# Optimization experiments

Hardware: AMD Instinct MI355X
Metric: run time of the kernel (lower is better)

Reference implementation:

```python
import jax, jax.numpy as jnp
import numpy as np

E, H, M, IN, T = 4, 64, 64, 32, 32      # e_size, hidden_state, message, in_size, target
HL = (128, 256, 128)                     # NNet hidden layers (priba's NNet default)
N_LAYERS = 3


def setup_inputs() -> dict:
    key = jax.random.key(0)
    ks = iter(jax.random.split(key, 64))
    B, N = 16, 128

    def w(shape, scale=0.1):
        return jax.random.normal(next(ks), shape, dtype=jnp.float32) * scale

    inp = {
        "h_in": jax.random.normal(next(ks), (B, N, IN), dtype=jnp.float32),
        "am": jax.random.normal(next(ks), (B, N, N, E), dtype=jnp.float32),
        "g_size": jax.random.randint(next(ks), (B,), 0, N),
    }
    # EdgeNetwork NNet: E -> 128 -> 256 -> 128 -> M*H
    dims_e = (E,) + HL + (M * H,)
    for i in range(4):
        inp[f"We{i}"] = w((dims_e[i], dims_e[i + 1]))
        inp[f"be{i}"] = w((dims_e[i + 1],))
    # GRU (torch nn.GRU, one layer, one step): input M, hidden H
    inp["Wih"] = w((3 * H, M)); inp["Whh"] = w((3 * H, H))
    inp["bih"] = w((3 * H,)); inp["bhh"] = w((3 * H,))
    # Readout NNets: i on [h_T, h_0] (H+IN -> T), j on h_T (H -> T)
    dims_i = (H + IN,) + HL + (T,)
    dims_j = (H,) + HL + (T,)
    for i in range(4):
        inp[f"Wi{i}"] = w((dims_i[i], dims_i[i + 1])); inp[f"bi{i}"] = w((dims_i[i + 1],))
        inp[f"Wj{i}"] = w((dims_j[i], dims_j[i + 1])); inp[f"bj{i}"] = w((dims_j[i + 1],))
    return inp


def _mlp(x, Ws, bs):
    for Wk, bk in zip(Ws[:-1], bs[:-1]):
        x = jax.nn.relu(x @ Wk + bk)
    return x @ Ws[-1] + bs[-1]


def reference(h_in, am, g_size,
              We0, be0, We1, be1, We2, be2, We3, be3,
              Wih, Whh, bih, bhh,
              Wi0, bi0, Wi1, bi1, Wi2, bi2, Wi3, bi3,
              Wj0, bj0, Wj1, bj1, Wj2, bj2, Wj3, bj3):
    B, N, _ = h_in.shape
    h = jnp.pad(h_in, ((0, 0), (0, 0), (0, H - IN)))            # pad to hidden size
    mask = (jnp.arange(N)[None, :] < g_size[:, None]).astype(h.dtype)[:, :, None]  # [B,N,1]

    # Edge-network hidden features; final linear layer is fused into the
    # message contraction to avoid materializing per-edge [M,H] matrices.
    f = am                                                       # [B,N,N,E]
    for Wk, bk in ((We0, be0), (We1, be1), (We2, be2)):
        f = jax.nn.relu(f @ Wk + bk)                             # [B,N,N,128]
    W3 = We3.reshape(HL[-1], M, H)                               # [128,M,H]
    b3 = be3.reshape(M, H)

    for _ in range(N_LAYERS):                                    # weight-tied GGNN steps
        # m[b,v,o] = sum_w (A(e_bvw) @ h_bw)[o], A = reshape(f @ We3 + be3)
        t = jnp.einsum('bvwk,bwi->bvki', f, h)                   # [B,N,128,H]
        msg = jnp.einsum('bvki,koi->bvo', t, W3)
        msg = msg + jnp.einsum('oi,bi->bo', b3, h.sum(1))[:, None, :]
        # single-step torch GRU update
        gi = msg @ Wih.T + bih
        gh = h @ Whh.T + bhh
        r = jax.nn.sigmoid(gi[..., :H] + gh[..., :H])
        z = jax.nn.sigmoid(gi[..., H:2 * H] + gh[..., H:2 * H])
        n = jnp.tanh(gi[..., 2 * H:] + r * gh[..., 2 * H:])
        h = (1.0 - z) * n + z * h
        h = h * mask

    # GGNN readout: sum_v mask * sigmoid(i([h_T, h_0])) * j(h_T), then log_softmax
    gate = jax.nn.sigmoid(_mlp(jnp.concatenate([h, h_in], -1),
                               (Wi0, Wi1, Wi2, Wi3), (bi0, bi1, bi2, bi3)))
    val = _mlp(h, (Wj0, Wj1, Wj2, Wj3), (bj0, bj1, bj2, bj3))
    res = (mask * gate * val).sum(1)                             # [B,T]
    return jax.nn.log_softmax(res, axis=1)
```

## Files before the change

### kernel.cpp

```cpp
#include <hip/hip_runtime.h>
#include <math.h>

#define B   16
#define N   128
#define E   4
#define H   64
#define M   64
#define IN_ 32
#define T   32
#define K1  128
#define K2  256
#define K3  128

typedef _Float16 f16;
typedef f16  f16x8 __attribute__((ext_vector_type(8)));
typedef f16  f16x4 __attribute__((ext_vector_type(4)));
typedef f16  f16x2 __attribute__((ext_vector_type(2)));
typedef float f32x4 __attribute__((ext_vector_type(4)));

#define MFMA16(a, b, c) __builtin_amdgcn_mfma_f32_16x16x32_f16(a, b, c, 0, 0, 0)

#define OFF_W1T   0
#define OFF_W2T   32768
#define OFF_WE3H  65536
#define OFF_RI0   589824
#define OFF_RI1   602112
#define OFF_RI2   634880
#define OFF_RI3   667648
#define OFF_RJ0   671744
#define OFF_RJ1   679936
#define OFF_RJ2   712704
#define OFF_RJ3   745472
#define WPACK_SZ  749568

union SmemU {
    struct { float xl[64][4]; f16 y1[64][136]; f16 y2[64][264]; } e;
    union {
        struct { f16 Al[128][72]; f16 Bl[128][72]; } in;
        f16 Ol[128][136];
    } pg;
    struct { float prt[4][64]; float hsum[64]; float bias[64]; } bi;
};

__global__ __launch_bounds__(256) void prep_kernel(
    const float* __restrict__ h_in,
    const float* __restrict__ We1, const float* __restrict__ We2,
    const float* __restrict__ We3,
    const float* __restrict__ Wi0, const float* __restrict__ Wi1,
    const float* __restrict__ Wi2, const float* __restrict__ Wi3,
    const float* __restrict__ Wj0, const float* __restrict__ Wj1,
    const float* __restrict__ Wj2, const float* __restrict__ Wj3,
    float* __restrict__ h, f16* __restrict__ h16, f16* __restrict__ hin16,
    f16* __restrict__ wp) {
    int idx = blockIdx.x * 256 + threadIdx.x;
    if (idx < B * N * H) {
        int i  = idx & (H - 1);
        int bn = idx >> 6;
        float v = (i < IN_) ? h_in[bn * IN_ + i] : 0.f;
        h[idx] = v;
        h16[idx] = (f16)v;
        if (i < IN_) hin16[bn * IN_ + i] = (f16)v;
    }
    if (idx >= WPACK_SZ) return;
    if (idx < OFF_W2T) {
        int j = idx >> 7, k = idx & 127;
        wp[idx] = (f16)We1[k * 256 + j];
    } else if (idx < OFF_WE3H) {
        int t = idx - OFF_W2T;
        int j = t >> 8, k = t & 255;
        wp[idx] = (f16)We2[k * 128 + j];
    } else if (idx < OFF_RI0) {
        wp[idx] = (f16)We3[idx - OFF_WE3H];
    } else if (idx < OFF_RI1) {
        int t = idx - OFF_RI0;
        int n = t / 96, c = t % 96;
        wp[idx] = (f16)Wi0[c * 128 + n];
    } else if (idx < OFF_RI2) {
        int t = idx - OFF_RI1;
        int n = t >> 7, k = t & 127;
        wp[idx] = (f16)Wi1[k * 256 + n];
    } else if (idx < OFF_RI3) {
        int t = idx - OFF_RI2;
        int n = t >> 8, k = t & 255;
        wp[idx] = (f16)Wi2[k * 128 + n];
    } else if (idx < OFF_RJ0) {
        int t = idx - OFF_RI3;
        int n = t >> 7, k = t & 127;
        wp[idx] = (f16)Wi3[k * 32 + n];
    } else if (idx < OFF_RJ1) {
        int t = idx - OFF_RJ0;
        int n = t >> 6, c = t & 63;
        wp[idx] = (f16)Wj0[c * 128 + n];
    } else if (idx < OFF_RJ2) {
        int t = idx - OFF_RJ1;
        int n = t >> 7, k = t & 127;
        wp[idx] = (f16)Wj1[k * 256 + n];
    } else if (idx < OFF_RJ3) {
        int t = idx - OFF_RJ2;
        int n = t >> 8, k = t & 255;
        wp[idx] = (f16)Wj2[k * 128 + n];
    } else {
        int t = idx - OFF_RJ3;
        int n = t >> 7, k = t & 127;
        wp[idx] = (f16)Wj3[k * 32 + n];
    }
}


__device__ void edge_body(SmemU& su, int tid, int tile,
                          const float* __restrict__ am,
                          const float* __restrict__ We0,
                          const float* __restrict__ be0,
                          const f16* __restrict__ W1t,
                          const float* __restrict__ be1,
                          const f16* __restrict__ W2t,
                          const float* __restrict__ be2,
                          f16* __restrict__ f) {
    int lane = tid & 63, wv = tid >> 6;
    long long g0 = (long long)tile * 64;

    ((float*)su.e.xl)[tid] = am[g0 * 4 + tid];
    __syncthreads();

    {
        int j0 = (tid & 63) * 2, e0 = (tid >> 6) * 16;
        float w00 = We0[j0],       w01 = We0[j0 + 1];
        float w10 = We0[128 + j0], w11 = We0[128 + j0 + 1];
        float w20 = We0[256 + j0], w21 = We0[256 + j0 + 1];
        float w30 = We0[384 + j0], w31 = We0[384 + j0 + 1];
        float b0 = be0[j0], b1 = be0[j0 + 1];
        #pragma unroll 4
        for (int e = e0; e < e0 + 16; ++e) {
            float x0 = su.e.xl[e][0], x1 = su.e.xl[e][1];
            float x2 = su.e.xl[e][2], x3 = su.e.xl[e][3];
            float v0 = b0 + x0 * w00 + x1 * w10 + x2 * w20 + x3 * w30;
            float v1 = b1 + x0 * w01 + x1 * w11 + x2 * w21 + x3 * w31;
            f16x2 p;
            p[0] = (f16)fmaxf(v0, 0.f);
            p[1] = (f16)fmaxf(v1, 0.f);
            *(f16x2*)&su.e.y1[e][j0] = p;
        }
    }
    __syncthreads();

    int m = lane & 15, q = lane >> 4;

    {
        f32x4 acc[4][4];
        #pragma unroll
        for (int ct = 0; ct < 4; ++ct)
            #pragma unroll
            for (int rt = 0; rt < 4; ++rt) acc[ct][rt] = (f32x4){0.f, 0.f, 0.f, 0.f};
        #pragma unroll
        for (int s = 0; s < 4; ++s) {
            int k0 = s * 32 + q * 8;
            f16x8 afr[4], bfr[4];
            #pragma unroll
            for (int rt = 0; rt < 4; ++rt)
                afr[rt] = *(const f16x8*)&su.e.y1[rt * 16 + m][k0];
            #pragma unroll
            for (int ct = 0; ct < 4; ++ct) {
                int n = (wv * 4 + ct) * 16 + m;
                bfr[ct] = *(const f16x8*)(W1t + n * 128 + k0);
            }
            #pragma unroll
            for (int ct = 0; ct < 4; ++ct)
                #pragma unroll
                for (int rt = 0; rt < 4; ++rt)
                    acc[ct][rt] = MFMA16(bfr[ct], afr[rt], acc[ct][rt]);
        }
        #pragma unroll
        for (int ct = 0; ct < 4; ++ct) {
            int n0 = (wv * 4 + ct) * 16 + q * 4;
            f32x4 bb = *(const f32x4*)&be1[n0];
            #pragma unroll
            for (int rt = 0; rt < 4; ++rt) {
                int e = rt * 16 + m;
                f16x4 pk;
                #pragma unroll
                for (int r = 0; r < 4; ++r)
                    pk[r] = (f16)fmaxf(acc[ct][rt][r] + bb[r], 0.f);
                *(f16x4*)&su.e.y2[e][n0] = pk;
            }
        }
    }
    __syncthreads();

    {
        f32x4 acc[2][4];
        #pragma unroll
        for (int ct = 0; ct < 2; ++ct)
            #pragma unroll
            for (int rt = 0; rt < 4; ++rt) acc[ct][rt] = (f32x4){0.f, 0.f, 0.f, 0.f};
        #pragma unroll
        for (int s = 0; s < 8; ++s) {
            int k0 = s * 32 + q * 8;
            f16x8 afr[4], bfr[2];
            #pragma unroll
            for (int rt = 0; rt < 4; ++rt)
                afr[rt] = *(const f16x8*)&su.e.y2[rt * 16 + m][k0];
            #pragma unroll
            for (int ct = 0; ct < 2; ++ct) {
                int n = (wv * 2 + ct) * 16 + m;
                bfr[ct] = *(const f16x8*)(W2t + n * 256 + k0);
            }
            #pragma unroll
            for (int ct = 0; ct < 2; ++ct)
                #pragma unroll
                for (int rt = 0; rt < 4; ++rt)
                    acc[ct][rt] = MFMA16(bfr[ct], afr[rt], acc[ct][rt]);
        }
        #pragma unroll
        for (int ct = 0; ct < 2; ++ct) {
            int n0 = (wv * 2 + ct) * 16 + q * 4;
            f32x4 bb = *(const f32x4*)&be2[n0];
            #pragma unroll
            for (int rt = 0; rt < 4; ++rt) {
                int e = rt * 16 + m;
                f16x4 pk;
                #pragma unroll
                for (int r = 0; r < 4; ++r)
                    pk[r] = (f16)fmaxf(acc[ct][rt][r] + bb[r], 0.f);
                *(f16x4*)&su.e.y1[e][n0] = pk;
            }
        }
    }
    __syncthreads();

    #pragma unroll
    for (int j = 0; j < 4; ++j) {
        int c = tid + j * 256;
        int e = c >> 4, pp = c & 15;
        *(uint4*)(f + (g0 + e) * 128 + pp * 8) = *(const uint4*)&su.e.y1[e][pp * 8];
    }
}

__device__ void pgemm_body(SmemU& su, int tid, int ob, int nt,
                           const f16* __restrict__ h16,
                           const f16* __restrict__ We3h,
                           f16* __restrict__ P2) {
    int lane = tid & 63, wv = tid >> 6;

    #pragma unroll
    for (int j = 0; j < 4; ++j) {
        int c = tid + j * 256;
        int row = c >> 3, pp = c & 7;
        *(uint4*)&su.pg.in.Al[row][pp * 8] =
            *(const uint4*)(h16 + (size_t)(nt * 128 + row) * 64 + pp * 8);
    }
    #pragma unroll
    for (int j = 0; j < 4; ++j) {
        int c = tid + j * 256;
        int k = c >> 3, pp = c & 7;
        *(uint4*)&su.pg.in.Bl[k][pp * 8] =
            *(const uint4*)(We3h + ((size_t)(k * 64 + ob)) * 64 + pp * 8);
    }
    __syncthreads();

    int m = lane & 15, q = lane >> 4;
    f32x4 acc[2][8];
    #pragma unroll
    for (int ct = 0; ct < 2; ++ct)
        #pragma unroll
        for (int rt = 0; rt < 8; ++rt) acc[ct][rt] = (f32x4){0.f, 0.f, 0.f, 0.f};
    #pragma unroll
    for (int s = 0; s < 2; ++s) {
        int k0 = s * 32 + q * 8;
        f16x8 afr[8], bfr[2];
        #pragma unroll
        for (int rt = 0; rt < 8; ++rt)
            afr[rt] = *(const f16x8*)&su.pg.in.Al[rt * 16 + m][k0];
        #pragma unroll
        for (int ct = 0; ct < 2; ++ct)
            bfr[ct] = *(const f16x8*)&su.pg.in.Bl[(wv * 2 + ct) * 16 + m][k0];
        #pragma unroll
        for (int ct = 0; ct < 2; ++ct)
            #pragma unroll
            for (int rt = 0; rt < 8; ++rt)
                acc[ct][rt] = MFMA16(bfr[ct], afr[rt], acc[ct][rt]);
    }
    __syncthreads();
    #pragma unroll
    for (int ct = 0; ct < 2; ++ct) {
        int c0 = (wv * 2 + ct) * 16 + q * 4;
        #pragma unroll
        for (int rt = 0; rt < 8; ++rt) {
            int v = rt * 16 + m;
            f16x4 pk;
            #pragma unroll
            for (int r = 0; r < 4; ++r) pk[r] = (f16)acc[ct][rt][r];
            *(f16x4*)&su.pg.Ol[v][c0] = pk;
        }
    }
    __syncthreads();
    #pragma unroll
    for (int j = 0; j < 8; ++j) {
        int c = tid + j * 256;
        int row = c >> 4, pp = c & 15;
        *(uint4*)(P2 + ((size_t)(nt * 128 + row) * 64 + ob) * 128 + pp * 8) =
            *(const uint4*)&su.pg.Ol[row][pp * 8];
    }
}

__device__ void bias_body(SmemU& su, int tid, int b,
                          const float* __restrict__ h,
                          const float* __restrict__ be3,
                          float* __restrict__ biasb) {
    int i = tid & 63, wq = tid >> 6;
    float s = 0.f;
    for (int w = wq; w < N; w += 4) s += h[((size_t)(b * N + w)) * H + i];
    su.bi.prt[wq][i] = s;
    __syncthreads();
    if (tid < 64)
        su.bi.hsum[tid] = su.bi.prt[0][tid] + su.bi.prt[1][tid]
                        + su.bi.prt[2][tid] + su.bi.prt[3][tid];
    __syncthreads();
    if (tid < 64) {
        float sb = 0.f;
        #pragma unroll 4
        for (int ii = 0; ii < H; ++ii) sb += be3[tid * H + ii] * su.bi.hsum[ii];
        biasb[b * 64 + tid] = sb;
    }
}

__global__ __launch_bounds__(256, 3) void mega0_kernel(
    const float* __restrict__ am,
    const float* __restrict__ We0, const float* __restrict__ be0,
    const float* __restrict__ be1, const float* __restrict__ be2,
    const float* __restrict__ be3,
    const f16* __restrict__ wp,
    const float* __restrict__ h, const f16* __restrict__ h16,
    f16* __restrict__ f, f16* __restrict__ P2, float* __restrict__ biasb) {
    __shared__ SmemU su;
    int tid = threadIdx.x;
    int bid = blockIdx.x;
    if (bid < 4096) {
        edge_body(su, tid, bid, am, We0, be0, wp + OFF_W1T, be1, wp + OFF_W2T,
                  be2, f);
    } else if (bid < 5120) {
        int t = bid - 4096;
        pgemm_body(su, tid, t & 63, t >> 6, h16, wp + OFF_WE3H, P2);
    } else {
        bias_body(su, tid, bid - 5120, h, be3, biasb);
    }
}

__global__ __launch_bounds__(256, 3) void pg_bias_kernel(
    const float* __restrict__ be3, const f16* __restrict__ wp,
    const float* __restrict__ h, const f16* __restrict__ h16,
    f16* __restrict__ P2, float* __restrict__ biasb) {
    __shared__ SmemU su;
    int tid = threadIdx.x;
    int bid = blockIdx.x;
    if (bid < 1024) {
        pgemm_body(su, tid, bid & 63, bid >> 6, h16, wp + OFF_WE3H, P2);
    } else {
        bias_body(su, tid, bid - 1024, h, be3, biasb);
    }
}

__global__ __launch_bounds__(256, 2) void msg_mfma(
    const f16* __restrict__ f, const f16* __restrict__ P2,
    float* __restrict__ part) {
    __shared__ f16 Al[128][136];
    __shared__ f16 Bl[64][136];
    int tid = threadIdx.x, lane = tid & 63, wv = tid >> 6;
    int ws = blockIdx.x;
    int b  = blockIdx.y;
    int m = lane & 15, q = lane >> 4;

    f32x4 acc[2][4];
    #pragma unroll
    for (int rt = 0; rt < 2; ++rt)
        #pragma unroll
        for (int ct = 0; ct < 4; ++ct) acc[rt][ct] = (f32x4){0.f, 0.f, 0.f, 0.f};

    for (int wi = 0; wi < 4; ++wi) {
        int w = ws * 4 + wi;
        #pragma unroll
        for (int j = 0; j < 8; ++j) {
            int c = tid + j * 256;
            int v = c >> 4, pp = c & 15;
            *(uint4*)&Al[v][pp * 8] =
                *(const uint4*)(f + (((size_t)(b * 128 + v) * 128 + w) * 128) + pp * 8);
        }
        #pragma unroll
        for (int j = 0; j < 4; ++j) {
            int c = tid + j * 256;
            int o = c >> 4, pp = c & 15;
            *(uint4*)&Bl[o][pp * 8] =
                *(const uint4*)(P2 + (((size_t)(b * 128 + w) * 64 + o) * 128) + pp * 8);
        }
        __syncthreads();
        #pragma unroll
        for (int s = 0; s < 4; ++s) {
            int k0 = s * 32 + q * 8;
            f16x8 afr[2], bfr[4];
            #pragma unroll
            for (int rt = 0; rt < 2; ++rt)
                afr[rt] = *(const f16x8*)&Al[(wv * 2 + rt) * 16 + m][k0];
            #pragma unroll
            for (int ct = 0; ct < 4; ++ct)
                bfr[ct] = *(const f16x8*)&Bl[ct * 16 + m][k0];
            #pragma unroll
            for (int rt = 0; rt < 2; ++rt)
                #pragma unroll
                for (int ct = 0; ct < 4; ++ct)
                    acc[rt][ct] = MFMA16(afr[rt], bfr[ct], acc[rt][ct]);
        }
        __syncthreads();
    }
    float* pp = part + (size_t)ws * (2048 * 64);
    #pragma unroll
    for (int rt = 0; rt < 2; ++rt)
        #pragma unroll
        for (int ct = 0; ct < 4; ++ct) {
            int o = ct * 16 + m;
            #pragma unroll
            for (int r = 0; r < 4; ++r) {
                int v = (wv * 2 + rt) * 16 + q * 4 + r;
                pp[(size_t)(b * 128 + v) * 64 + o] = acc[rt][ct][r];
            }
        }
}

__global__ __launch_bounds__(192) void gru_kernel(
    const float* __restrict__ biasb, const float* __restrict__ part,
    float* __restrict__ h, f16* __restrict__ h16,
    const float* __restrict__ Wih, const float* __restrict__ Whh,
    const float* __restrict__ bih, const float* __restrict__ bhh,
    const int* __restrict__ g_size) {
    __shared__ float m_lds[M];
    __shared__ float h_lds[H];
    __shared__ float gi[3 * H], gh[3 * H];
    int tid = threadIdx.x;
    int bv  = blockIdx.x;
    int b = bv >> 7, v = bv & 127;

    if (tid < M) {
        float s = biasb[b * 64 + tid];
        #pragma unroll 8
        for (int sp = 0; sp < 32; ++sp)
            s += part[(size_t)sp * (2048 * 64) + bv * 64 + tid];
        m_lds[tid] = s;
    } else if (tid < M + H) {
        h_lds[tid - M] = h[bv * H + (tid - M)];
    }
    __syncthreads();

    {
        float si = bih[tid], sh = bhh[tid];
        const float* wi = Wih + tid * M;
        const float* wh = Whh + tid * H;
        #pragma unroll 4
        for (int k = 0; k < M; ++k) si += wi[k] * m_lds[k];
        #pragma unroll 4
        for (int k = 0; k < H; ++k) sh += wh[k] * h_lds[k];
        gi[tid] = si;
        gh[tid] = sh;
    }
    __syncthreads();
    if (tid < H) {
        float r = 1.f / (1.f + expf(-(gi[tid] + gh[tid])));
        float z = 1.f / (1.f + expf(-(gi[H + tid] + gh[H + tid])));
        float n = tanhf(gi[2 * H + tid] + r * gh[2 * H + tid]);
        float hv = (1.f - z) * n + z * h_lds[tid];
        float maskf = (v < g_size[b]) ? 1.f : 0.f;
        hv *= maskf;
        h[bv * H + tid] = hv;
        h16[bv * H + tid] = (f16)hv;
    }
}

__global__ __launch_bounds__(256, 4) void readout_mfma(
    const f16* __restrict__ h16, const f16* __restrict__ hin16,
    const int* __restrict__ g_size, const f16* __restrict__ wp,
    const float* __restrict__ bi0, const float* __restrict__ bi1,
    const float* __restrict__ bi2, const float* __restrict__ bi3,
    const float* __restrict__ bj0, const float* __restrict__ bj1,
    const float* __restrict__ bj2, const float* __restrict__ bj3,
    float* __restrict__ contrib) {
    __shared__ f16 Xl[32][104];
    __shared__ f16 A1[32][136];
    __shared__ f16 A2[32][264];
    __shared__ float Gl[32][36];
    const f16* Ri0 = wp + OFF_RI0; const f16* Ri1 = wp + OFF_RI1;
    const f16* Ri2 = wp + OFF_RI2; const f16* Ri3 = wp + OFF_RI3;
    const f16* Rj0 = wp + OFF_RJ0; const f16* Rj1 = wp + OFF_RJ1;
    const f16* Rj2 = wp + OFF_RJ2; const f16* Rj3 = wp + OFF_RJ3;
    int tid = threadIdx.x, lane = tid & 63, wv = tid >> 6;
    int m = lane & 15, q = lane >> 4;
    int r0 = blockIdx.x * 32;

    {
        int row = tid >> 3, pp = tid & 7;
        *(uint4*)&Xl[row][pp * 8] = *(const uint4*)(h16 + (size_t)(r0 + row) * 64 + pp * 8);
        if (tid < 128) {
            int row2 = tid >> 2, p2 = tid & 3;
            *(uint4*)&Xl[row2][64 + p2 * 8] =
                *(const uint4*)(hin16 + (size_t)(r0 + row2) * 32 + p2 * 8);
        }
    }
    __syncthreads();

    {
        f32x4 acc[2][2];
        #pragma unroll
        for (int ct = 0; ct < 2; ++ct)
            #pragma unroll
            for (int rt = 0; rt < 2; ++rt) acc[ct][rt] = (f32x4){0.f, 0.f, 0.f, 0.f};
        #pragma unroll
        for (int s = 0; s < 3; ++s) {
            int k0 = s * 32 + q * 8;
            f16x8 afr[2], bfr[2];
            #pragma unroll
            for (int rt = 0; rt < 2; ++rt) afr[rt] = *(const f16x8*)&Xl[rt * 16 + m][k0];
            #pragma unroll
            for (int ct = 0; ct < 2; ++ct)
                bfr[ct] = *(const f16x8*)(Ri0 + ((wv * 2 + ct) * 16 + m) * 96 + k0);
            #pragma unroll
            for (int ct = 0; ct < 2; ++ct)
                #pragma unroll
                for (int rt = 0; rt < 2; ++rt)
                    acc[ct][rt] = MFMA16(afr[rt], bfr[ct], acc[ct][rt]);
        }
        #pragma unroll
        for (int ct = 0; ct < 2; ++ct) {
            int n = (wv * 2 + ct) * 16 + m;
            float bb = bi0[n];
            #pragma unroll
            for (int rt = 0; rt < 2; ++rt)
                #pragma unroll
                for (int r = 0; r < 4; ++r)
                    A1[rt * 16 + q * 4 + r][n] = (f16)fmaxf(acc[ct][rt][r] + bb, 0.f);
        }
    }
    __syncthreads();

    {
        f32x4 acc[4][2];
        #pragma unroll
        for (int ct = 0; ct < 4; ++ct)
            #pragma unroll
            for (int rt = 0; rt < 2; ++rt) acc[ct][rt] = (f32x4){0.f, 0.f, 0.f, 0.f};
        #pragma unroll
        for (int s = 0; s < 4; ++s) {
            int k0 = s * 32 + q * 8;
            f16x8 afr[2], bfr[4];
            #pragma unroll
            for (int rt = 0; rt < 2; ++rt) afr[rt] = *(const f16x8*)&A1[rt * 16 + m][k0];
            #pragma unroll
            for (int ct = 0; ct < 4; ++ct)
                bfr[ct] = *(const f16x8*)(Ri1 + ((wv * 4 + ct) * 16 + m) * 128 + k0);
            #pragma unroll
            for (int ct = 0; ct < 4; ++ct)
                #pragma unroll
                for (int rt = 0; rt < 2; ++rt)
                    acc[ct][rt] = MFMA16(afr[rt], bfr[ct], acc[ct][rt]);
        }
        #pragma unroll
        for (int ct = 0; ct < 4; ++ct) {
            int n = (wv * 4 + ct) * 16 + m;
            float bb = bi1[n];
            #pragma unroll
            for (int rt = 0; rt < 2; ++rt)
                #pragma unroll
                for (int r = 0; r < 4; ++r)
                    A2[rt * 16 + q * 4 + r][n] = (f16)fmaxf(acc[ct][rt][r] + bb, 0.f);
        }
    }
    __syncthreads();

    {
        f32x4 acc[2][2];
        #pragma unroll
        for (int ct = 0; ct < 2; ++ct)
            #pragma unroll
            for (int rt = 0; rt < 2; ++rt) acc[ct][rt] = (f32x4){0.f, 0.f, 0.f, 0.f};
        #pragma unroll
        for (int s = 0; s < 8; ++s) {
            int k0 = s * 32 + q * 8;
            f16x8 afr[2], bfr[2];
            #pragma unroll
            for (int rt = 0; rt < 2; ++rt) afr[rt] = *(const f16x8*)&A2[rt * 16 + m][k0];
            #pragma unroll
            for (int ct = 0; ct < 2; ++ct)
                bfr[ct] = *(const f16x8*)(Ri2 + ((wv * 2 + ct) * 16 + m) * 256 + k0);
            #pragma unroll
            for (int ct = 0; ct < 2; ++ct)
                #pragma unroll
                for (int rt = 0; rt < 2; ++rt)
                    acc[ct][rt] = MFMA16(afr[rt], bfr[ct], acc[ct][rt]);
        }
        __syncthreads();
        #pragma unroll
        for (int ct = 0; ct < 2; ++ct) {
            int n = (wv * 2 + ct) * 16 + m;
            float bb = bi2[n];
            #pragma unroll
            for (int rt = 0; rt < 2; ++rt)
                #pragma unroll
                for (int r = 0; r < 4; ++r)
                    A1[rt * 16 + q * 4 + r][n] = (f16)fmaxf(acc[ct][rt][r] + bb, 0.f);
        }
    }
    __syncthreads();

    if (wv < 2) {
        f32x4 acc[2];
        acc[0] = (f32x4){0.f, 0.f, 0.f, 0.f};
        acc[1] = (f32x4){0.f, 0.f, 0.f, 0.f};
        int n = wv * 16 + m;
        #pragma unroll
        for (int s = 0; s < 4; ++s) {
            int k0 = s * 32 + q * 8;
            f16x8 bfr = *(const f16x8*)(Ri3 + n * 128 + k0);
            #pragma unroll
            for (int rt = 0; rt < 2; ++rt) {
                f16x8 afr = *(const f16x8*)&A1[rt * 16 + m][k0];
                acc[rt] = MFMA16(afr, bfr, acc[rt]);
            }
        }
        float bb = bi3[n];
        #pragma unroll
        for (int rt = 0; rt < 2; ++rt)
            #pragma unroll
            for (int r = 0; r < 4; ++r)
                Gl[rt * 16 + q * 4 + r][n] = 1.f / (1.f + expf(-(acc[rt][r] + bb)));
    }
    __syncthreads();

    {
        f32x4 acc[2][2];
        #pragma unroll
        for (int ct = 0; ct < 2; ++ct)
            #pragma unroll
            for (int rt = 0; rt < 2; ++rt) acc[ct][rt] = (f32x4){0.f, 0.f, 0.f, 0.f};
        #pragma unroll
        for (int s = 0; s < 2; ++s) {
            int k0 = s * 32 + q * 8;
            f16x8 afr[2], bfr[2];
            #pragma unroll
            for (int rt = 0; rt < 2; ++rt) afr[rt] = *(const f16x8*)&Xl[rt * 16 + m][k0];
            #pragma unroll
            for (int ct = 0; ct < 2; ++ct)
                bfr[ct] = *(const f16x8*)(Rj0 + ((wv * 2 + ct) * 16 + m) * 64 + k0);
            #pragma unroll
            for (int ct = 0; ct < 2; ++ct)
                #pragma unroll
                for (int rt = 0; rt < 2; ++rt)
                    acc[ct][rt] = MFMA16(afr[rt], bfr[ct], acc[ct][rt]);
        }
        __syncthreads();
        #pragma unroll
        for (int ct = 0; ct < 2; ++ct) {
            int n = (wv * 2 + ct) * 16 + m;
            float bb = bj0[n];
            #pragma unroll
            for (int rt = 0; rt < 2; ++rt)
                #pragma unroll
                for (int r = 0; r < 4; ++r)
                    A1[rt * 16 + q * 4 + r][n] = (f16)fmaxf(acc[ct][rt][r] + bb, 0.f);
        }
    }
    __syncthreads();

    {
        f32x4 acc[4][2];
        #pragma unroll
        for (int ct = 0; ct < 4; ++ct)
            #pragma unroll
            for (int rt = 0; rt < 2; ++rt) acc[ct][rt] = (f32x4){0.f, 0.f, 0.f, 0.f};
        #pragma unroll
        for (int s = 0; s < 4; ++s) {
            int k0 = s * 32 + q * 8;
            f16x8 afr[2], bfr[4];
            #pragma unroll
            for (int rt = 0; rt < 2; ++rt) afr[rt] = *(const f16x8*)&A1[rt * 16 + m][k0];
            #pragma unroll
            for (int ct = 0; ct < 4; ++ct)
                bfr[ct] = *(const f16x8*)(Rj1 + ((wv * 4 + ct) * 16 + m) * 128 + k0);
            #pragma unroll
            for (int ct = 0; ct < 4; ++ct)
                #pragma unroll
                for (int rt = 0; rt < 2; ++rt)
                    acc[ct][rt] = MFMA16(afr[rt], bfr[ct], acc[ct][rt]);
        }
        #pragma unroll
        for (int ct = 0; ct < 4; ++ct) {
            int n = (wv * 4 + ct) * 16 + m;
            float bb = bj1[n];
            #pragma unroll
            for (int rt = 0; rt < 2; ++rt)
                #pragma unroll
                for (int r = 0; r < 4; ++r)
                    A2[rt * 16 + q * 4 + r][n] = (f16)fmaxf(acc[ct][rt][r] + bb, 0.f);
        }
    }
    __syncthreads();

    {
        f32x4 acc[2][2];
        #pragma unroll
        for (int ct = 0; ct < 2; ++ct)
            #pragma unroll
            for (int rt = 0; rt < 2; ++rt) acc[ct][rt] = (f32x4){0.f, 0.f, 0.f, 0.f};
        #pragma unroll
        for (int s = 0; s < 8; ++s) {
            int k0 = s * 32 + q * 8;
            f16x8 afr[2], bfr[2];
            #pragma unroll
            for (int rt = 0; rt < 2; ++rt) afr[rt] = *(const f16x8*)&A2[rt * 16 + m][k0];
            #pragma unroll
            for (int ct = 0; ct < 2; ++ct)
                bfr[ct] = *(const f16x8*)(Rj2 + ((wv * 2 + ct) * 16 + m) * 256 + k0);
            #pragma unroll
            for (int ct = 0; ct < 2; ++ct)
                #pragma unroll
                for (int rt = 0; rt < 2; ++rt)
                    acc[ct][rt] = MFMA16(afr[rt], bfr[ct], acc[ct][rt]);
        }
        __syncthreads();
        #pragma unroll
        for (int ct = 0; ct < 2; ++ct) {
            int n = (wv * 2 + ct) * 16 + m;
            float bb = bj2[n];
            #pragma unroll
            for (int rt = 0; rt < 2; ++rt)
                #pragma unroll
                for (int r = 0; r < 4; ++r)
                    A1[rt * 16 + q * 4 + r][n] = (f16)fmaxf(acc[ct][rt][r] + bb, 0.f);
        }
    }
    __syncthreads();

    if (wv < 2) {
        f32x4 acc[2];
        acc[0] = (f32x4){0.f, 0.f, 0.f, 0.f};
        acc[1] = (f32x4){0.f, 0.f, 0.f, 0.f};
        int n = wv * 16 + m;
        #pragma unroll
        for (int s = 0; s < 4; ++s) {
            int k0 = s * 32 + q * 8;
            f16x8 bfr = *(const f16x8*)(Rj3 + n * 128 + k0);
            #pragma unroll
            for (int rt = 0; rt < 2; ++rt) {
                f16x8 afr = *(const f16x8*)&A1[rt * 16 + m][k0];
                acc[rt] = MFMA16(afr, bfr, acc[rt]);
            }
        }
        float bb = bj3[n];
        #pragma unroll
        for (int rt = 0; rt < 2; ++rt)
            #pragma unroll
            for (int r = 0; r < 4; ++r) {
                int row = rt * 16 + q * 4 + r;
                int rg = r0 + row;
                int b = rg >> 7, v = rg & 127;
                float maskf = (v < g_size[b]) ? 1.f : 0.f;
                contrib[(size_t)rg * T + n] = maskf * Gl[row][n] * (acc[rt][r] + bb);
            }
    }
}

__global__ __launch_bounds__(64) void finalize_kernel(const float* __restrict__ contrib,
                                                      float* __restrict__ out) {
    __shared__ float res[T];
    int b = blockIdx.x;
    int o = threadIdx.x;
    if (o < T) {
        float s = 0.f;
        for (int v = 0; v < N; ++v) s += contrib[(b * N + v) * T + o];
        res[o] = s;
    }
    __syncthreads();
    if (o < T) {
        float mx = res[0];
        for (int i = 1; i < T; ++i) mx = fmaxf(mx, res[i]);
        float se = 0.f;
        for (int i = 0; i < T; ++i) se += expf(res[i] - mx);
        out[b * T + o] = res[o] - mx - logf(se);
    }
}

extern "C" void kernel_launch(void* const* d_in, const int* in_sizes, int n_in,
                              void* d_out, int out_size, void* d_ws, size_t ws_size,
                              hipStream_t stream) {
    (void)in_sizes; (void)n_in; (void)out_size; (void)ws_size;
    const float* h_in = (const float*)d_in[0];
    const float* am   = (const float*)d_in[1];
    const int*   g_sz = (const int*)d_in[2];
    const float* We0 = (const float*)d_in[3],  *be0 = (const float*)d_in[4];
    const float* We1 = (const float*)d_in[5],  *be1 = (const float*)d_in[6];
    const float* We2 = (const float*)d_in[7],  *be2 = (const float*)d_in[8];
    const float* We3 = (const float*)d_in[9],  *be3 = (const float*)d_in[10];
    const float* Wih = (const float*)d_in[11], *Whh = (const float*)d_in[12];
    const float* bih = (const float*)d_in[13], *bhh = (const float*)d_in[14];
    const float* Wi0 = (const float*)d_in[15], *bi0 = (const float*)d_in[16];
    const float* Wj0 = (const float*)d_in[17], *bj0 = (const float*)d_in[18];
    const float* Wi1 = (const float*)d_in[19], *bi1 = (const float*)d_in[20];
    const float* Wj1 = (const float*)d_in[21], *bj1 = (const float*)d_in[22];
    const float* Wi2 = (const float*)d_in[23], *bi2 = (const float*)d_in[24];
    const float* Wj2 = (const float*)d_in[25], *bj2 = (const float*)d_in[26];
    const float* Wi3 = (const float*)d_in[27], *bi3 = (const float*)d_in[28];
    const float* Wj3 = (const float*)d_in[29], *bj3 = (const float*)d_in[30];

    float* out = (float*)d_out;

    f16*   f    = (f16*)d_ws;
    f16*   P2   = f + (size_t)33554432;
    float* part = (float*)(P2 + (size_t)16777216);
    float* h    = part + (size_t)4194304;
    float* biasb = h + 131072;
    float* contrib = biasb + 1024;
    f16*   h16  = (f16*)(contrib + 65536);
    f16*   hin16 = h16 + 131072;
    f16*   wp   = hin16 + 65536;

    prep_kernel<<<(WPACK_SZ + 255) / 256, 256, 0, stream>>>(
        h_in, We1, We2, We3, Wi0, Wi1, Wi2, Wi3, Wj0, Wj1, Wj2, Wj3,
        h, h16, hin16, wp);

    mega0_kernel<<<4096 + 1024 + 16, 256, 0, stream>>>(
        am, We0, be0, be1, be2, be3, wp, h, h16, f, P2, biasb);
    msg_mfma<<<dim3(32, 16), 256, 0, stream>>>(f, P2, part);
    gru_kernel<<<B * N, 192, 0, stream>>>(biasb, part, h, h16,
                                          Wih, Whh, bih, bhh, g_sz);

    for (int l = 1; l < 3; ++l) {
        pg_bias_kernel<<<1024 + 16, 256, 0, stream>>>(be3, wp, h, h16, P2, biasb);
        msg_mfma<<<dim3(32, 16), 256, 0, stream>>>(f, P2, part);
        gru_kernel<<<B * N, 192, 0, stream>>>(biasb, part, h, h16,
                                              Wih, Whh, bih, bhh, g_sz);
    }

    readout_mfma<<<64, 256, 0, stream>>>(h16, hin16, g_sz, wp,
                                         bi0, bi1, bi2, bi3,
                                         bj0, bj1, bj2, bj3, contrib);
    finalize_kernel<<<B, 64, 0, stream>>>(contrib, out);
}
```

Baseline: 398.1 us.

## Double block size in edge/pgemm kernels and halve readout row tile

Edge MLP, P-GEMM and bias kernels move from 256 to 512 threads per block, with the per-wave work split halved (8 waves instead of 4). The readout kernel handles 16 rows per block instead of 32, so it launches twice as many blocks. The aim is more waves in flight and better CU coverage for the small readout grid. The cost is that each MFMA B fragment is reused across fewer tiles, so there are more global and LDS fragment loads per FLOP, and the larger blocks may pressure register limits.

```diff
diff --git a/kernel.cpp b/kernel.cpp
--- a/kernel.cpp
+++ b/kernel.cpp
@@ -39,7 +39,7 @@
         struct { f16 Al[128][72]; f16 Bl[128][72]; } in;
         f16 Ol[128][136];
     } pg;
-    struct { float prt[4][64]; float hsum[64]; float bias[64]; } bi;
+    struct { float prt[8][64]; float hsum[64]; float bias[64]; } bi;
 };
 
 __global__ __launch_bounds__(256) void prep_kernel(
@@ -119,18 +119,18 @@
     int lane = tid & 63, wv = tid >> 6;
     long long g0 = (long long)tile * 64;
 
-    ((float*)su.e.xl)[tid] = am[g0 * 4 + tid];
-    __syncthreads();
-
-    {
-        int j0 = (tid & 63) * 2, e0 = (tid >> 6) * 16;
+    if (tid < 256) ((float*)su.e.xl)[tid] = am[g0 * 4 + tid];
+    __syncthreads();
+
+    {
+        int j0 = (tid & 63) * 2, e0 = (tid >> 6) * 8;
         float w00 = We0[j0],       w01 = We0[j0 + 1];
         float w10 = We0[128 + j0], w11 = We0[128 + j0 + 1];
         float w20 = We0[256 + j0], w21 = We0[256 + j0 + 1];
         float w30 = We0[384 + j0], w31 = We0[384 + j0 + 1];
         float b0 = be0[j0], b1 = be0[j0 + 1];
         #pragma unroll 4
-        for (int e = e0; e < e0 + 16; ++e) {
+        for (int e = e0; e < e0 + 8; ++e) {
             float x0 = su.e.xl[e][0], x1 = su.e.xl[e][1];
             float x2 = su.e.xl[e][2], x3 = su.e.xl[e][3];
             float v0 = b0 + x0 * w00 + x1 * w10 + x2 * w20 + x3 * w30;
@@ -146,32 +146,32 @@
     int m = lane & 15, q = lane >> 4;
 
     {
-        f32x4 acc[4][4];
-        #pragma unroll
-        for (int ct = 0; ct < 4; ++ct)
+        f32x4 acc[2][4];
+        #pragma unroll
+        for (int ct = 0; ct < 2; ++ct)
             #pragma unroll
             for (int rt = 0; rt < 4; ++rt) acc[ct][rt] = (f32x4){0.f, 0.f, 0.f, 0.f};
         #pragma unroll
         for (int s = 0; s < 4; ++s) {
             int k0 = s * 32 + q * 8;
-            f16x8 afr[4], bfr[4];
+            f16x8 afr[4], bfr[2];
             #pragma unroll
             for (int rt = 0; rt < 4; ++rt)
                 afr[rt] = *(const f16x8*)&su.e.y1[rt * 16 + m][k0];
             #pragma unroll
-            for (int ct = 0; ct < 4; ++ct) {
-                int n = (wv * 4 + ct) * 16 + m;
+            for (int ct = 0; ct < 2; ++ct) {
+                int n = (wv * 2 + ct) * 16 + m;
                 bfr[ct] = *(const f16x8*)(W1t + n * 128 + k0);
             }
             #pragma unroll
-            for (int ct = 0; ct < 4; ++ct)
+            for (int ct = 0; ct < 2; ++ct)
                 #pragma unroll
                 for (int rt = 0; rt < 4; ++rt)
                     acc[ct][rt] = MFMA16(bfr[ct], afr[rt], acc[ct][rt]);
         }
         #pragma unroll
-        for (int ct = 0; ct < 4; ++ct) {
-            int n0 = (wv * 4 + ct) * 16 + q * 4;
+        for (int ct = 0; ct < 2; ++ct) {
+            int n0 = (wv * 2 + ct) * 16 + q * 4;
             f32x4 bb = *(const f32x4*)&be1[n0];
             #pragma unroll
             for (int rt = 0; rt < 4; ++rt) {
@@ -187,49 +187,37 @@
     __syncthreads();
 
     {
-        f32x4 acc[2][4];
-        #pragma unroll
-        for (int ct = 0; ct < 2; ++ct)
-            #pragma unroll
-            for (int rt = 0; rt < 4; ++rt) acc[ct][rt] = (f32x4){0.f, 0.f, 0.f, 0.f};
+        f32x4 acc[4];
+        #pragma unroll
+        for (int rt = 0; rt < 4; ++rt) acc[rt] = (f32x4){0.f, 0.f, 0.f, 0.f};
+        int n = wv * 16 + m;
         #pragma unroll
         for (int s = 0; s < 8; ++s) {
             int k0 = s * 32 + q * 8;
-            f16x8 afr[4], bfr[2];
-            #pragma unroll
-            for (int rt = 0; rt < 4; ++rt)
-                afr[rt] = *(const f16x8*)&su.e.y2[rt * 16 + m][k0];
-            #pragma unroll
-            for (int ct = 0; ct < 2; ++ct) {
-                int n = (wv * 2 + ct) * 16 + m;
-                bfr[ct] = *(const f16x8*)(W2t + n * 256 + k0);
-            }
-            #pragma unroll
-            for (int ct = 0; ct < 2; ++ct)
-                #pragma unroll
-                for (int rt = 0; rt < 4; ++rt)
-                    acc[ct][rt] = MFMA16(bfr[ct], afr[rt], acc[ct][rt]);
-        }
-        #pragma unroll
-        for (int ct = 0; ct < 2; ++ct) {
-            int n0 = (wv * 2 + ct) * 16 + q * 4;
-            f32x4 bb = *(const f32x4*)&be2[n0];
+            f16x8 bfr = *(const f16x8*)(W2t + n * 256 + k0);
             #pragma unroll
             for (int rt = 0; rt < 4; ++rt) {
-                int e = rt * 16 + m;
-                f16x4 pk;
-                #pragma unroll
-                for (int r = 0; r < 4; ++r)
-                    pk[r] = (f16)fmaxf(acc[ct][rt][r] + bb[r], 0.f);
-                *(f16x4*)&su.e.y1[e][n0] = pk;
-            }
+                f16x8 afr = *(const f16x8*)&su.e.y2[rt * 16 + m][k0];
+                acc[rt] = MFMA16(bfr, afr, acc[rt]);
+            }
+        }
+        int n0 = wv * 16 + q * 4;
+        f32x4 bb = *(const f32x4*)&be2[n0];
+        #pragma unroll
+        for (int rt = 0; rt < 4; ++rt) {
+            int e = rt * 16 + m;
+            f16x4 pk;
+            #pragma unroll
+            for (int r = 0; r < 4; ++r)
+                pk[r] = (f16)fmaxf(acc[rt][r] + bb[r], 0.f);
+            *(f16x4*)&su.e.y1[e][n0] = pk;
         }
     }
     __syncthreads();
 
     #pragma unroll
-    for (int j = 0; j < 4; ++j) {
-        int c = tid + j * 256;
+    for (int j = 0; j < 2; ++j) {
+        int c = tid + j * 512;
         int e = c >> 4, pp = c & 15;
         *(uint4*)(f + (g0 + e) * 128 + pp * 8) = *(const uint4*)&su.e.y1[e][pp * 8];
     }
@@ -242,15 +230,15 @@
     int lane = tid & 63, wv = tid >> 6;
 
     #pragma unroll
-    for (int j = 0; j < 4; ++j) {
-        int c = tid + j * 256;
+    for (int j = 0; j < 2; ++j) {
+        int c = tid + j * 512;
         int row = c >> 3, pp = c & 7;
         *(uint4*)&su.pg.in.Al[row][pp * 8] =
             *(const uint4*)(h16 + (size_t)(nt * 128 + row) * 64 + pp * 8);
     }
     #pragma unroll
-    for (int j = 0; j < 4; ++j) {
-        int c = tid + j * 256;
+    for (int j = 0; j < 2; ++j) {
+        int c = tid + j * 512;
         int k = c >> 3, pp = c & 7;
         *(uint4*)&su.pg.in.Bl[k][pp * 8] =
             *(const uint4*)(We3h + ((size_t)(k * 64 + ob)) * 64 + pp * 8);
@@ -258,44 +246,37 @@
     __syncthreads();
 
     int m = lane & 15, q = lane >> 4;
-    f32x4 acc[2][8];
+    f32x4 acc[8];
     #pragma unroll
-    for (int ct = 0; ct < 2; ++ct)
-        #pragma unroll
-        for (int rt = 0; rt < 8; ++rt) acc[ct][rt] = (f32x4){0.f, 0.f, 0.f, 0.f};
+    for (int rt = 0; rt < 8; ++rt) acc[rt] = (f32x4){0.f, 0.f, 0.f, 0.f};
     #pragma unroll
     for (int s = 0; s < 2; ++s) {
         int k0 = s * 32 + q * 8;
-        f16x8 afr[8], bfr[2];
+        f16x8 afr[8];
         #pragma unroll
         for (int rt = 0; rt < 8; ++rt)
             afr[rt] = *(const f16x8*)&su.pg.in.Al[rt * 16 + m][k0];
-        #pragma unroll
-        for (int ct = 0; ct < 2; ++ct)
-            bfr[ct] = *(const f16x8*)&su.pg.in.Bl[(wv * 2 + ct) * 16 + m][k0];
-        #pragma unroll
-        for (int ct = 0; ct < 2; ++ct)
-            #pragma unroll
-            for (int rt = 0; rt < 8; ++rt)
-                acc[ct][rt] = MFMA16(bfr[ct], afr[rt], acc[ct][rt]);
-    }
-    __syncthreads();
-    #pragma unroll
-    for (int ct = 0; ct < 2; ++ct) {
-        int c0 = (wv * 2 + ct) * 16 + q * 4;
+        f16x8 bfr = *(const f16x8*)&su.pg.in.Bl[wv * 16 + m][k0];
+        #pragma unroll
+        for (int rt = 0; rt < 8; ++rt)
+            acc[rt] = MFMA16(bfr, afr[rt], acc[rt]);
+    }
+    __syncthreads();
+    {
+        int c0 = wv * 16 + q * 4;
         #pragma unroll
         for (int rt = 0; rt < 8; ++rt) {
             int v = rt * 16 + m;
             f16x4 pk;
             #pragma unroll
-            for (int r = 0; r < 4; ++r) pk[r] = (f16)acc[ct][rt][r];
+            for (int r = 0; r < 4; ++r) pk[r] = (f16)acc[rt][r];
             *(f16x4*)&su.pg.Ol[v][c0] = pk;
         }
     }
     __syncthreads();
     #pragma unroll
-    for (int j = 0; j < 8; ++j) {
-        int c = tid + j * 256;
+    for (int j = 0; j < 4; ++j) {
+        int c = tid + j * 512;
         int row = c >> 4, pp = c & 15;
         *(uint4*)(P2 + ((size_t)(nt * 128 + row) * 64 + ob) * 128 + pp * 8) =
             *(const uint4*)&su.pg.Ol[row][pp * 8];
@@ -308,12 +289,15 @@
                           float* __restrict__ biasb) {
     int i = tid & 63, wq = tid >> 6;
     float s = 0.f;
-    for (int w = wq; w < N; w += 4) s += h[((size_t)(b * N + w)) * H + i];
+    for (int w = wq; w < N; w += 8) s += h[((size_t)(b * N + w)) * H + i];
     su.bi.prt[wq][i] = s;
     __syncthreads();
-    if (tid < 64)
-        su.bi.hsum[tid] = su.bi.prt[0][tid] + su.bi.prt[1][tid]
-                        + su.bi.prt[2][tid] + su.bi.prt[3][tid];
+    if (tid < 64) {
+        float t = 0.f;
+        #pragma unroll
+        for (int p = 0; p < 8; ++p) t += su.bi.prt[p][tid];
+        su.bi.hsum[tid] = t;
+    }
     __syncthreads();
     if (tid < 64) {
         float sb = 0.f;
@@ -323,7 +307,7 @@
     }
 }
 
-__global__ __launch_bounds__(256, 3) void mega0_kernel(
+__global__ __launch_bounds__(512, 6) void mega0_kernel(
     const float* __restrict__ am,
     const float* __restrict__ We0, const float* __restrict__ be0,
     const float* __restrict__ be1, const float* __restrict__ be2,
@@ -345,7 +329,7 @@
     }
 }
 
-__global__ __launch_bounds__(256, 3) void pg_bias_kernel(
+__global__ __launch_bounds__(512, 6) void pg_bias_kernel(
     const float* __restrict__ be3, const f16* __restrict__ wp,
     const float* __restrict__ h, const f16* __restrict__ h16,
     f16* __restrict__ P2, float* __restrict__ biasb) {
@@ -480,22 +464,25 @@
     const float* __restrict__ bj0, const float* __restrict__ bj1,
     const float* __restrict__ bj2, const float* __restrict__ bj3,
     float* __restrict__ contrib) {
-    __shared__ f16 Xl[32][104];
-    __shared__ f16 A1[32][136];
-    __shared__ f16 A2[32][264];
-    __shared__ float Gl[32][36];
+    __shared__ f16 Xl[16][104];
+    __shared__ f16 A1[16][136];
+    __shared__ f16 A2[16][264];
+    __shared__ float Gl[16][36];
     const f16* Ri0 = wp + OFF_RI0; const f16* Ri1 = wp + OFF_RI1;
     const f16* Ri2 = wp + OFF_RI2; const f16* Ri3 = wp + OFF_RI3;
     const f16* Rj0 = wp + OFF_RJ0; const f16* Rj1 = wp + OFF_RJ1;
     const f16* Rj2 = wp + OFF_RJ2; const f16* Rj3 = wp + OFF_RJ3;
     int tid = threadIdx.x, lane = tid & 63, wv = tid >> 6;
     int m = lane & 15, q = lane >> 4;
-    int r0 = blockIdx.x * 32;
-
-    {
-        int row = tid >> 3, pp = tid & 7;
-        *(uint4*)&Xl[row][pp * 8] = *(const uint4*)(h16 + (size_t)(r0 + row) * 64 + pp * 8);
+    int r0 = blockIdx.x * 16;
+
+    {
         if (tid < 128) {
+            int row = tid >> 3, pp = tid & 7;
+            *(uint4*)&Xl[row][pp * 8] =
+                *(const uint4*)(h16 + (size_t)(r0 + row) * 64 + pp * 8);
+        }
+        if (tid < 64) {
             int row2 = tid >> 2, p2 = tid & 3;
             *(uint4*)&Xl[row2][64 + p2 * 8] =
                 *(const uint4*)(hin16 + (size_t)(r0 + row2) * 32 + p2 * 8);
@@ -504,93 +491,68 @@
     __syncthreads();
 
     {
-        f32x4 acc[2][2];
-        #pragma unroll
-        for (int ct = 0; ct < 2; ++ct)
-            #pragma unroll
-            for (int rt = 0; rt < 2; ++rt) acc[ct][rt] = (f32x4){0.f, 0.f, 0.f, 0.f};
+        f32x4 acc[2];
+        acc[0] = (f32x4){0.f, 0.f, 0.f, 0.f};
+        acc[1] = (f32x4){0.f, 0.f, 0.f, 0.f};
         #pragma unroll
         for (int s = 0; s < 3; ++s) {
             int k0 = s * 32 + q * 8;
-            f16x8 afr[2], bfr[2];
-            #pragma unroll
-            for (int rt = 0; rt < 2; ++rt) afr[rt] = *(const f16x8*)&Xl[rt * 16 + m][k0];
-            #pragma unroll
-            for (int ct = 0; ct < 2; ++ct)
-                bfr[ct] = *(const f16x8*)(Ri0 + ((wv * 2 + ct) * 16 + m) * 96 + k0);
-            #pragma unroll
-            for (int ct = 0; ct < 2; ++ct)
-                #pragma unroll
-                for (int rt = 0; rt < 2; ++rt)
-                    acc[ct][rt] = MFMA16(afr[rt], bfr[ct], acc[ct][rt]);
+            f16x8 afr = *(const f16x8*)&Xl[m][k0];
+            #pragma unroll
+            for (int ct = 0; ct < 2; ++ct) {
+                f16x8 bfr = *(const f16x8*)(Ri0 + ((wv * 2 + ct) * 16 + m) * 96 + k0);
+                acc[ct] = MFMA16(afr, bfr, acc[ct]);
+            }
         }
         #pragma unroll
         for (int ct = 0; ct < 2; ++ct) {
             int n = (wv * 2 + ct) * 16 + m;
             float bb = bi0[n];
             #pragma unroll
-            for (int rt = 0; rt < 2; ++rt)
-                #pragma unroll
-                for (int r = 0; r < 4; ++r)
-                    A1[rt * 16 + q * 4 + r][n] = (f16)fmaxf(acc[ct][rt][r] + bb, 0.f);
-        }
-    }
-    __syncthreads();
-
-    {
-        f32x4 acc[4][2];
-        #pragma unroll
-        for (int ct = 0; ct < 4; ++ct)
-            #pragma unroll
-            for (int rt = 0; rt < 2; ++rt) acc[ct][rt] = (f32x4){0.f, 0.f, 0.f, 0.f};
+            for (int r = 0; r < 4; ++r)
+                A1[q * 4 + r][n] = (f16)fmaxf(acc[ct][r] + bb, 0.f);
+        }
+    }
+    __syncthreads();
+
+    {
+        f32x4 acc[4];
+        #pragma unroll
+        for (int ct = 0; ct < 4; ++ct) acc[ct] = (f32x4){0.f, 0.f, 0.f, 0.f};
         #pragma unroll
         for (int s = 0; s < 4; ++s) {
             int k0 = s * 32 + q * 8;
-            f16x8 afr[2], bfr[4];
-            #pragma unroll
-            for (int rt = 0; rt < 2; ++rt) afr[rt] = *(const f16x8*)&A1[rt * 16 + m][k0];
-            #pragma unroll
-            for (int ct = 0; ct < 4; ++ct)
-                bfr[ct] = *(const f16x8*)(Ri1 + ((wv * 4 + ct) * 16 + m) * 128 + k0);
-            #pragma unroll
-            for (int ct = 0; ct < 4; ++ct)
-                #pragma unroll
-                for (int rt = 0; rt < 2; ++rt)
-                    acc[ct][rt] = MFMA16(afr[rt], bfr[ct], acc[ct][rt]);
+            f16x8 afr = *(const f16x8*)&A1[m][k0];
+            #pragma unroll
+            for (int ct = 0; ct < 4; ++ct) {
+                f16x8 bfr = *(const f16x8*)(Ri1 + ((wv * 4 + ct) * 16 + m) * 128 + k0);
+                acc[ct] = MFMA16(afr, bfr, acc[ct]);
+            }
         }
         #pragma unroll
         for (int ct = 0; ct < 4; ++ct) {
             int n = (wv * 4 + ct) * 16 + m;
             float bb = bi1[n];
             #pragma unroll
-            for (int rt = 0; rt < 2; ++rt)
-                #pragma unroll
-                for (int r = 0; r < 4; ++r)
-                    A2[rt * 16 + q * 4 + r][n] = (f16)fmaxf(acc[ct][rt][r] + bb, 0.f);
-        }
-    }
-    __syncthreads();
-
-    {
-        f32x4 acc[2][2];
-        #pragma unroll
-        for (int ct = 0; ct < 2; ++ct)
-            #pragma unroll
-            for (int rt = 0; rt < 2; ++rt) acc[ct][rt] = (f32x4){0.f, 0.f, 0.f, 0.f};
+            for (int r = 0; r < 4; ++r)
+                A2[q * 4 + r][n] = (f16)fmaxf(acc[ct][r] + bb, 0.f);
+        }
+    }
+    __syncthreads();
+
+    {
+        f32x4 acc[2];
+        acc[0] = (f32x4){0.f, 0.f, 0.f, 0.f};
+        acc[1] = (f32x4){0.f, 0.f, 0.f, 0.f};
         #pragma unroll
         for (int s = 0; s < 8; ++s) {
             int k0 = s * 32 + q * 8;
-            f16x8 afr[2], bfr[2];
-            #pragma unroll
-            for (int rt = 0; rt < 2; ++rt) afr[rt] = *(const f16x8*)&A2[rt * 16 + m][k0];
-            #pragma unroll
-            for (int ct = 0; ct < 2; ++ct)
-                bfr[ct] = *(const f16x8*)(Ri2 + ((wv * 2 + ct) * 16 + m) * 256 + k0);
-            #pragma unroll
-            for (int ct = 0; ct < 2; ++ct)
-                #pragma unroll
-                for (int rt = 0; rt < 2; ++rt)
-                    acc[ct][rt] = MFMA16(afr[rt], bfr[ct], acc[ct][rt]);
+            f16x8 afr = *(const f16x8*)&A2[m][k0];
+            #pragma unroll
+            for (int ct = 0; ct < 2; ++ct) {
+                f16x8 bfr = *(const f16x8*)(Ri2 + ((wv * 2 + ct) * 16 + m) * 256 + k0);
+                acc[ct] = MFMA16(afr, bfr, acc[ct]);
+            }
         }
         __syncthreads();
         #pragma unroll
@@ -598,58 +560,42 @@
             int n = (wv * 2 + ct) * 16 + m;
             float bb = bi2[n];
             #pragma unroll
-            for (int rt = 0; rt < 2; ++rt)
-                #pragma unroll
-                for (int r = 0; r < 4; ++r)
-                    A1[rt * 16 + q * 4 + r][n] = (f16)fmaxf(acc[ct][rt][r] + bb, 0.f);
+            for (int r = 0; r < 4; ++r)
+                A1[q * 4 + r][n] = (f16)fmaxf(acc[ct][r] + bb, 0.f);
         }
     }
     __syncthreads();
 
     if (wv < 2) {
+        f32x4 acc = (f32x4){0.f, 0.f, 0.f, 0.f};
+        int n = wv * 16 + m;
+        #pragma unroll
+        for (int s = 0; s < 4; ++s) {
+            int k0 = s * 32 + q * 8;
+            f16x8 bfr = *(const f16x8*)(Ri3 + n * 128 + k0);
+            f16x8 afr = *(const f16x8*)&A1[m][k0];
+            acc = MFMA16(afr, bfr, acc);
+        }
+        float bb = bi3[n];
+        #pragma unroll
+        for (int r = 0; r < 4; ++r)
+            Gl[q * 4 + r][n] = 1.f / (1.f + expf(-(acc[r] + bb)));
+    }
+    __syncthreads();
+
+    {
         f32x4 acc[2];
         acc[0] = (f32x4){0.f, 0.f, 0.f, 0.f};
         acc[1] = (f32x4){0.f, 0.f, 0.f, 0.f};
-        int n = wv * 16 + m;
-        #pragma unroll
-        for (int s = 0; s < 4; ++s) {
-            int k0 = s * 32 + q * 8;
-            f16x8 bfr = *(const f16x8*)(Ri3 + n * 128 + k0);
-            #pragma unroll
-            for (int rt = 0; rt < 2; ++rt) {
-                f16x8 afr = *(const f16x8*)&A1[rt * 16 + m][k0];
-                acc[rt] = MFMA16(afr, bfr, acc[rt]);
-            }
-        }
-        float bb = bi3[n];
-        #pragma unroll
-        for (int rt = 0; rt < 2; ++rt)
-            #pragma unroll
-            for (int r = 0; r < 4; ++r)
-                Gl[rt * 16 + q * 4 + r][n] = 1.f / (1.f + expf(-(acc[rt][r] + bb)));
-    }
-    __syncthreads();
-
-    {
-        f32x4 acc[2][2];
-        #pragma unroll
-        for (int ct = 0; ct < 2; ++ct)
-            #pragma unroll
-            for (int rt = 0; rt < 2; ++rt) acc[ct][rt] = (f32x4){0.f, 0.f, 0.f, 0.f};
         #pragma unroll
         for (int s = 0; s < 2; ++s) {
             int k0 = s * 32 + q * 8;
-            f16x8 afr[2], bfr[2];
-            #pragma unroll
-            for (int rt = 0; rt < 2; ++rt) afr[rt] = *(const f16x8*)&Xl[rt * 16 + m][k0];
-            #pragma unroll
-            for (int ct = 0; ct < 2; ++ct)
-                bfr[ct] = *(const f16x8*)(Rj0 + ((wv * 2 + ct) * 16 + m) * 64 + k0);
-            #pragma unroll
-            for (int ct = 0; ct < 2; ++ct)
-                #pragma unroll
-                for (int rt = 0; rt < 2; ++rt)
-                    acc[ct][rt] = MFMA16(afr[rt], bfr[ct], acc[ct][rt]);
+            f16x8 afr = *(const f16x8*)&Xl[m][k0];
+            #pragma unroll
+            for (int ct = 0; ct < 2; ++ct) {
+                f16x8 bfr = *(const f16x8*)(Rj0 + ((wv * 2 + ct) * 16 + m) * 64 + k0);
+                acc[ct] = MFMA16(afr, bfr, acc[ct]);
+            }
         }
         __syncthreads();
         #pragma unroll
@@ -657,68 +603,50 @@
             int n = (wv * 2 + ct) * 16 + m;
             float bb = bj0[n];
             #pragma unroll
-            for (int rt = 0; rt < 2; ++rt)
-                #pragma unroll
-                for (int r = 0; r < 4; ++r)
-                    A1[rt * 16 + q * 4 + r][n] = (f16)fmaxf(acc[ct][rt][r] + bb, 0.f);
-        }
-    }
-    __syncthreads();
-
-    {
-        f32x4 acc[4][2];
-        #pragma unroll
-        for (int ct = 0; ct < 4; ++ct)
-            #pragma unroll
-            for (int rt = 0; rt < 2; ++rt) acc[ct][rt] = (f32x4){0.f, 0.f, 0.f, 0.f};
+            for (int r = 0; r < 4; ++r)
+                A1[q * 4 + r][n] = (f16)fmaxf(acc[ct][r] + bb, 0.f);
+        }
+    }
+    __syncthreads();
+
+    {
+        f32x4 acc[4];
+        #pragma unroll
+        for (int ct = 0; ct < 4; ++ct) acc[ct] = (f32x4){0.f, 0.f, 0.f, 0.f};
         #pragma unroll
         for (int s = 0; s < 4; ++s) {
             int k0 = s * 32 + q * 8;
-            f16x8 afr[2], bfr[4];
-            #pragma unroll
-            for (int rt = 0; rt < 2; ++rt) afr[rt] = *(const f16x8*)&A1[rt * 16 + m][k0];
-            #pragma unroll
-            for (int ct = 0; ct < 4; ++ct)
-                bfr[ct] = *(const f16x8*)(Rj1 + ((wv * 4 + ct) * 16 + m) * 128 + k0);
-            #pragma unroll
-            for (int ct = 0; ct < 4; ++ct)
-                #pragma unroll
-                for (int rt = 0; rt < 2; ++rt)
-                    acc[ct][rt] = MFMA16(afr[rt], bfr[ct], acc[ct][rt]);
+            f16x8 afr = *(const f16x8*)&A1[m][k0];
+            #pragma unroll
+            for (int ct = 0; ct < 4; ++ct) {
+                f16x8 bfr = *(const f16x8*)(Rj1 + ((wv * 4 + ct) * 16 + m) * 128 + k0);
+                acc[ct] = MFMA16(afr, bfr, acc[ct]);
+            }
         }
         #pragma unroll
         for (int ct = 0; ct < 4; ++ct) {
             int n = (wv * 4 + ct) * 16 + m;
             float bb = bj1[n];
             #pragma unroll
-            for (int rt = 0; rt < 2; ++rt)
-                #pragma unroll
-                for (int r = 0; r < 4; ++r)
-                    A2[rt * 16 + q * 4 + r][n] = (f16)fmaxf(acc[ct][rt][r] + bb, 0.f);
-        }
-    }
-    __syncthreads();
-
-    {
-        f32x4 acc[2][2];
-        #pragma unroll
-        for (int ct = 0; ct < 2; ++ct)
-            #pragma unroll
-            for (int rt = 0; rt < 2; ++rt) acc[ct][rt] = (f32x4){0.f, 0.f, 0.f, 0.f};
+            for (int r = 0; r < 4; ++r)
+                A2[q * 4 + r][n] = (f16)fmaxf(acc[ct][r] + bb, 0.f);
+        }
+    }
+    __syncthreads();
+
+    {
+        f32x4 acc[2];
+        acc[0] = (f32x4){0.f, 0.f, 0.f, 0.f};
+        acc[1] = (f32x4){0.f, 0.f, 0.f, 0.f};
         #pragma unroll
         for (int s = 0; s < 8; ++s) {
             int k0 = s * 32 + q * 8;
-            f16x8 afr[2], bfr[2];
-            #pragma unroll
-            for (int rt = 0; rt < 2; ++rt) afr[rt] = *(const f16x8*)&A2[rt * 16 + m][k0];
-            #pragma unroll
-            for (int ct = 0; ct < 2; ++ct)
-                bfr[ct] = *(const f16x8*)(Rj2 + ((wv * 2 + ct) * 16 + m) * 256 + k0);
-            #pragma unroll
-            for (int ct = 0; ct < 2; ++ct)
-                #pragma unroll
-                for (int rt = 0; rt < 2; ++rt)
-                    acc[ct][rt] = MFMA16(afr[rt], bfr[ct], acc[ct][rt]);
+            f16x8 afr = *(const f16x8*)&A2[m][k0];
+            #pragma unroll
+            for (int ct = 0; ct < 2; ++ct) {
+                f16x8 bfr = *(const f16x8*)(Rj2 + ((wv * 2 + ct) * 16 + m) * 256 + k0);
+                acc[ct] = MFMA16(afr, bfr, acc[ct]);
+            }
         }
         __syncthreads();
         #pragma unroll
@@ -726,40 +654,31 @@
             int n = (wv * 2 + ct) * 16 + m;
             float bb = bj2[n];
             #pragma unroll
-            for (int rt = 0; rt < 2; ++rt)
-                #pragma unroll
-                for (int r = 0; r < 4; ++r)
-                    A1[rt * 16 + q * 4 + r][n] = (f16)fmaxf(acc[ct][rt][r] + bb, 0.f);
+            for (int r = 0; r < 4; ++r)
+                A1[q * 4 + r][n] = (f16)fmaxf(acc[ct][r] + bb, 0.f);
         }
     }
     __syncthreads();
 
     if (wv < 2) {
-        f32x4 acc[2];
-        acc[0] = (f32x4){0.f, 0.f, 0.f, 0.f};
-        acc[1] = (f32x4){0.f, 0.f, 0.f, 0.f};
+        f32x4 acc = (f32x4){0.f, 0.f, 0.f, 0.f};
         int n = wv * 16 + m;
         #pragma unroll
         for (int s = 0; s < 4; ++s) {
             int k0 = s * 32 + q * 8;
             f16x8 bfr = *(const f16x8*)(Rj3 + n * 128 + k0);
-            #pragma unroll
-            for (int rt = 0; rt < 2; ++rt) {
-                f16x8 afr = *(const f16x8*)&A1[rt * 16 + m][k0];
-                acc[rt] = MFMA16(afr, bfr, acc[rt]);
-            }
+            f16x8 afr = *(const f16x8*)&A1[m][k0];
+            acc = MFMA16(afr, bfr, acc);
         }
         float bb = bj3[n];
         #pragma unroll
-        for (int rt = 0; rt < 2; ++rt)
-            #pragma unroll
-            for (int r = 0; r < 4; ++r) {
-                int row = rt * 16 + q * 4 + r;
-                int rg = r0 + row;
-                int b = rg >> 7, v = rg & 127;
-                float maskf = (v < g_size[b]) ? 1.f : 0.f;
-                contrib[(size_t)rg * T + n] = maskf * Gl[row][n] * (acc[rt][r] + bb);
-            }
+        for (int r = 0; r < 4; ++r) {
+            int row = q * 4 + r;
+            int rg = r0 + row;
+            int b = rg >> 7, v = rg & 127;
+            float maskf = (v < g_size[b]) ? 1.f : 0.f;
+            contrib[(size_t)rg * T + n] = maskf * Gl[row][n] * (acc[r] + bb);
+        }
     }
 }
 
@@ -821,21 +740,21 @@
         h_in, We1, We2, We3, Wi0, Wi1, Wi2, Wi3, Wj0, Wj1, Wj2, Wj3,
         h, h16, hin16, wp);
 
-    mega0_kernel<<<4096 + 1024 + 16, 256, 0, stream>>>(
+    mega0_kernel<<<4096 + 1024 + 16, 512, 0, stream>>>(
         am, We0, be0, be1, be2, be3, wp, h, h16, f, P2, biasb);
     msg_mfma<<<dim3(32, 16), 256, 0, stream>>>(f, P2, part);
     gru_kernel<<<B * N, 192, 0, stream>>>(biasb, part, h, h16,
                                           Wih, Whh, bih, bhh, g_sz);
 
     for (int l = 1; l < 3; ++l) {
-        pg_bias_kernel<<<1024 + 16, 256, 0, stream>>>(be3, wp, h, h16, P2, biasb);
+        pg_bias_kernel<<<1024 + 16, 512, 0, stream>>>(be3, wp, h, h16, P2, biasb);
         msg_mfma<<<dim3(32, 16), 256, 0, stream>>>(f, P2, part);
         gru_kernel<<<B * N, 192, 0, stream>>>(biasb, part, h, h16,
                                               Wih, Whh, bih, bhh, g_sz);
     }
 
-    readout_mfma<<<64, 256, 0, stream>>>(h16, hin16, g_sz, wp,
-                                         bi0, bi1, bi2, bi3,
-                                         bj0, bj1, bj2, bj3, contrib);
+    readout_mfma<<<128, 256, 0, stream>>>(h16, hin16, g_sz, wp,
+                                          bi0, bi1, bi2, bi3,
+                                          bj0, bj1, bj2, bj3, contrib);
     finalize_kernel<<<B, 64, 0, stream>>>(contrib, out);
 }
```

Result: slower. 419.7 us (+5.4%).
